# Kernel tuning notes

Hardware: AMD Instinct MI355X
Metric: run time of the kernel (lower is better)

The kernel has to match this reference:

```python
import jax, jax.numpy as jnp
import numpy as np

EMBED_DIM = 64
NUM_HEADS = 8
D_K = EMBED_DIM // NUM_HEADS  # 8
B, S = 8, 1024


def setup_inputs() -> dict:
    key = jax.random.key(0)
    ks = jax.random.split(key, 10)
    f32 = jnp.float32
    lim = 1.0 / np.sqrt(EMBED_DIM)
    def lin(k):
        kw, kb = jax.random.split(k)
        w = jax.random.uniform(kw, (EMBED_DIM, EMBED_DIM), f32, -lim, lim)
        b = jax.random.uniform(kb, (EMBED_DIM,), f32, -lim, lim)
        return w, b
    wq, bq = lin(ks[0])
    wk, bk = lin(ks[1])
    wv, bv = lin(ks[2])
    wo, bo = lin(ks[3])
    theta = jax.random.normal(ks[4], (EMBED_DIM,), f32)  # trainable RY angles, one per wire
    x = jax.random.normal(ks[5], (B, S, EMBED_DIM), f32)
    return {"x": x, "wq": wq, "bq": bq, "wk": wk, "bk": bk,
            "wv": wv, "bv": bv, "theta": theta, "wo": wo, "bo": bo}


def _quantum_map(t, theta):
    # Per-qubit circuit on |0>: RX(t_i) encode, RY(theta_i), <PauliZ_i>.
    # Product state => <Z_i> = cos(theta_i) * cos(t_i) exactly.
    return jnp.cos(theta) * jnp.cos(t.reshape(-1, EMBED_DIM))  # [N, E]


def reference(x, wq, bq, wk, bk, wv, bv, theta, wo, bo):
    # Linear QKV (torch nn.Linear: x @ W^T + b)
    q = x @ wq.T + bq
    k = x @ wk.T + bk
    v = x @ wv.T + bv
    # Quantum measurement map, flattened over batch*seq (as in the original)
    q_q = _quantum_map(q, theta)  # [N, E], N = B*S
    k_q = _quantum_map(k, theta)
    v_q = _quantum_map(v, theta)
    # Full flattened attention: [N, N] scores (original never reshapes back)
    scores = (q_q @ k_q.T) / jnp.sqrt(jnp.asarray(D_K, x.dtype))
    attn = jax.nn.softmax(scores, axis=-1)  # dropout is identity in eval
    out = attn @ v_q  # [N, E]
    return out @ wo.T + bo
```

## Files before the change

kernel.cpp:

```cpp
#include <hip/hip_runtime.h>
#include <hip/hip_bf16.h>

#define NQ 8192
#define DIM 64
#define SPLITS 8
#define QBLK 128
#define BN 64
#define KEYS_PER_SPLIT (NQ / SPLITS)
#define NTILES (KEYS_PER_SPLIT / BN)
#define SCALE 0.35355339059327373f
#define SC2   0.51012301920911057f

#define KSTR 72
#define VSTR 68

typedef short s8v __attribute__((ext_vector_type(8)));
typedef short s4v __attribute__((ext_vector_type(4)));
typedef float f4v __attribute__((ext_vector_type(4)));

__device__ __forceinline__ float b2f(short s) {
  unsigned int u = ((unsigned int)(unsigned short)s) << 16;
  return __uint_as_float(u);
}
__device__ __forceinline__ short f2b(float f) {
  __hip_bfloat16 h = __float2bfloat16(f);
  return *reinterpret_cast<short*>(&h);
}

__device__ __forceinline__ f4v mfma16(s4v a, s4v b, f4v c) {
#if __has_builtin(__builtin_amdgcn_mfma_f32_16x16x16bf16_1k)
  return __builtin_amdgcn_mfma_f32_16x16x16bf16_1k(a, b, c, 0, 0, 0);
#else
  f4v d;
  asm volatile("v_mfma_f32_16x16x16_bf16 %0, %1, %2, %3"
               : "=v"(d) : "v"(a), "v"(b), "v"(c));
  return d;
#endif
}

#define QROWS 16
__global__ __launch_bounds__(256) void qkv_kernel(
    const float* __restrict__ x,
    const float* __restrict__ wq, const float* __restrict__ bq,
    const float* __restrict__ wk, const float* __restrict__ bk,
    const float* __restrict__ wv, const float* __restrict__ bv,
    const float* __restrict__ theta,
    short* __restrict__ qq, short* __restrict__ kq, short* __restrict__ vq) {
  __shared__ __align__(16) short wsh[3][DIM][KSTR];
  __shared__ __align__(16) short xsb[QROWS][DIM];
  int tid = threadIdx.x;
  for (int i = tid; i < 3 * DIM * 16; i += 256) {
    int m = i >> 10;
    int rem = i & 1023;
    int r = rem >> 4, c4 = (rem & 15) << 2;
    const float* src = (m == 0) ? wq : (m == 1) ? wk : wv;
    float4 w = *(const float4*)&src[r * DIM + c4];
    s4v p = {f2b(w.x), f2b(w.y), f2b(w.z), f2b(w.w)};
    *(s4v*)&wsh[m][r][c4] = p;
  }
  int rowbase = blockIdx.x * QROWS;
  for (int i = tid; i < QROWS * 16; i += 256) {
    int r = i >> 4, c4 = (i & 15) << 2;
    float4 v = *(const float4*)&x[(rowbase + r) * DIM + c4];
    s4v p = {f2b(v.x), f2b(v.y), f2b(v.z), f2b(v.w)};
    *(s4v*)&xsb[r][c4] = p;
  }
  __syncthreads();
  int e = tid & 63, rg = tid >> 6;
  float ct = __cosf(theta[e]);
  float bqv = bq[e], bkv = bk[e], bvv = bv[e];
  for (int r = rg; r < QROWS; r += 4) {
    float aq = bqv, ak = bkv, av = bvv;
#pragma unroll
    for (int c8 = 0; c8 < 8; ++c8) {
      s8v xv = *(const s8v*)&xsb[r][c8 * 8];
      s8v w0 = *(const s8v*)&wsh[0][e][c8 * 8];
      s8v w1 = *(const s8v*)&wsh[1][e][c8 * 8];
      s8v w2 = *(const s8v*)&wsh[2][e][c8 * 8];
#pragma unroll
      for (int j = 0; j < 8; ++j) {
        float xf = b2f(xv[j]);
        aq += xf * b2f(w0[j]);
        ak += xf * b2f(w1[j]);
        av += xf * b2f(w2[j]);
      }
    }
    int n = rowbase + r;
    qq[n * DIM + e] = f2b(ct * __cosf(aq));
    kq[n * DIM + e] = f2b(ct * __cosf(ak));
    vq[n * DIM + e] = f2b(ct * __cosf(av));
  }
}

__global__ __launch_bounds__(256) void flash_kernel(
    const short* __restrict__ qq, const short* __restrict__ kq,
    const short* __restrict__ vq,
    float* __restrict__ pO, float* __restrict__ pL) {
  __shared__ __align__(16) short ksh[BN * KSTR];
  __shared__ __align__(16) short vsh[DIM * VSTR];

  int tid = threadIdx.x;
  int wave = tid >> 6, lane = tid & 63;
  int l15 = lane & 15, quad = lane >> 4;
  int qblock = blockIdx.x >> 3, split = blockIdx.x & 7;
  int qbase = qblock * QBLK + wave * 32;

  s8v qf[2][2];
#pragma unroll
  for (int qt = 0; qt < 2; ++qt) {
    const short* qr = qq + (qbase + qt * 16 + l15) * DIM + quad * 8;
    qf[qt][0] = *(const s8v*)qr;
    qf[qt][1] = *(const s8v*)(qr + 32);
  }

  f4v o[2][4];
  float ls[2] = {0.f, 0.f};
#pragma unroll
  for (int qt = 0; qt < 2; ++qt)
#pragma unroll
    for (int c = 0; c < 4; ++c) o[qt][c] = (f4v){0.f, 0.f, 0.f, 0.f};

  int kp = tid & 31, dch = tid >> 5;

  int kstart = split * KEYS_PER_SPLIT;
  for (int t = 0; t < NTILES; ++t) {
    int kbase = kstart + t * BN;
    __syncthreads();
    for (int i = tid; i < 512; i += 256) {
      int key = i >> 3, c8 = (i & 7) << 3;
      *(s8v*)&ksh[key * KSTR + c8] = *(const s8v*)&kq[(kbase + key) * DIM + c8];
    }
    {
      s8v r0 = *(const s8v*)&vq[(kbase + 2 * kp) * DIM + (dch << 3)];
      s8v r1 = *(const s8v*)&vq[(kbase + 2 * kp + 1) * DIM + (dch << 3)];
#pragma unroll
      for (int j = 0; j < 8; ++j) {
        int d = (dch << 3) + j;
        int pk = (int)(unsigned short)r0[j] | ((int)(unsigned short)r1[j] << 16);
        *(int*)&vsh[d * VSTR + 2 * kp] = pk;
      }
    }
    __syncthreads();

#pragma unroll
    for (int kt = 0; kt < 4; ++kt) {
      const short* kr = &ksh[(kt * 16 + l15) * KSTR + quad * 8];
      s8v kf0 = *(const s8v*)kr;
      s8v kf1 = *(const s8v*)(kr + 32);
      s4v pa[2];
#pragma unroll
      for (int qt = 0; qt < 2; ++qt) {
        f4v acc = (f4v){0.f, 0.f, 0.f, 0.f};
        acc = __builtin_amdgcn_mfma_f32_16x16x32_bf16(kf0, qf[qt][0], acc, 0, 0, 0);
        acc = __builtin_amdgcn_mfma_f32_16x16x32_bf16(kf1, qf[qt][1], acc, 0, 0, 0);
        s4v a;
        float sum = 0.f;
#pragma unroll
        for (int r = 0; r < 4; ++r) {
          float p = exp2f(acc[r] * SC2);
          short pb = f2b(p);
          a[r] = pb;
          sum += b2f(pb);
        }
        pa[qt] = a;
        ls[qt] += sum;
      }
#pragma unroll
      for (int c = 0; c < 4; ++c) {
        s4v vf = *(const s4v*)&vsh[(c * 16 + l15) * VSTR + kt * 16 + quad * 4];
#pragma unroll
        for (int qt = 0; qt < 2; ++qt)
          o[qt][c] = mfma16(pa[qt], vf, o[qt][c]);
      }
    }
  }

#pragma unroll
  for (int qt = 0; qt < 2; ++qt) {
    float v = ls[qt];
    v += __shfl_xor(v, 16);
    v += __shfl_xor(v, 32);
    ls[qt] = v;
  }

#pragma unroll
  for (int qt = 0; qt < 2; ++qt) {
#pragma unroll
    for (int r = 0; r < 4; ++r) {
      int q = qbase + qt * 16 + quad * 4 + r;
#pragma unroll
      for (int c = 0; c < 4; ++c)
        pO[((size_t)split * NQ + q) * DIM + c * 16 + l15] = o[qt][c][r];
    }
    if (quad == 0) pL[split * NQ + qbase + qt * 16 + l15] = ls[qt];
  }
}

#define MROWS 8
__global__ __launch_bounds__(256) void merge_kernel(
    const float* __restrict__ pO, const float* __restrict__ pL,
    const float* __restrict__ wo, const float* __restrict__ bo,
    float* __restrict__ out) {
  __shared__ __align__(16) short wsh[DIM][KSTR];
  __shared__ __align__(16) float att[MROWS][DIM];
  int tid = threadIdx.x;
  for (int i = tid; i < DIM * 16; i += 256) {
    int r = i >> 4, c4 = (i & 15) << 2;
    float4 w = *(const float4*)&wo[r * DIM + c4];
    s4v p = {f2b(w.x), f2b(w.y), f2b(w.z), f2b(w.w)};
    *(s4v*)&wsh[r][c4] = p;
  }
  int e = tid & 63, rg = tid >> 6;
  int q0 = blockIdx.x * MROWS;
  for (int rr = rg; rr < MROWS; rr += 4) {
    int q = q0 + rr;
    float s = 0.f, l = 0.f;
#pragma unroll
    for (int sp = 0; sp < SPLITS; ++sp) {
      s += pO[((size_t)sp * NQ + q) * DIM + e];
      l += pL[sp * NQ + q];
    }
    att[rr][e] = s / l;
  }
  __syncthreads();
  for (int rr = rg; rr < MROWS; rr += 4) {
    float acc = bo[e];
#pragma unroll
    for (int c8 = 0; c8 < 8; ++c8) {
      s8v w = *(const s8v*)&wsh[e][c8 * 8];
      float4 a0 = *(const float4*)&att[rr][c8 * 8];
      float4 a1 = *(const float4*)&att[rr][c8 * 8 + 4];
      acc += a0.x * b2f(w[0]) + a0.y * b2f(w[1]) + a0.z * b2f(w[2]) + a0.w * b2f(w[3])
           + a1.x * b2f(w[4]) + a1.y * b2f(w[5]) + a1.z * b2f(w[6]) + a1.w * b2f(w[7]);
    }
    out[(q0 + rr) * DIM + e] = acc;
  }
}

extern "C" void kernel_launch(void* const* d_in, const int* in_sizes, int n_in,
                              void* d_out, int out_size, void* d_ws, size_t ws_size,
                              hipStream_t stream) {
  const float* x  = (const float*)d_in[0];
  const float* wq = (const float*)d_in[1];
  const float* bq = (const float*)d_in[2];
  const float* wk = (const float*)d_in[3];
  const float* bk = (const float*)d_in[4];
  const float* wv = (const float*)d_in[5];
  const float* bv = (const float*)d_in[6];
  const float* th = (const float*)d_in[7];
  const float* wo = (const float*)d_in[8];
  const float* bo = (const float*)d_in[9];

  char* ws = (char*)d_ws;
  short* qq = (short*)(ws);
  short* kq = (short*)(ws + (1u << 20));
  short* vq = (short*)(ws + (2u << 20));
  float* pO = (float*)(ws + (3u << 20));
  float* pL = (float*)(ws + (3u << 20) + (size_t)SPLITS * NQ * DIM * 4);

  hipLaunchKernelGGL(qkv_kernel, dim3(NQ / QROWS), dim3(256), 0, stream,
                     x, wq, bq, wk, bk, wv, bv, th, qq, kq, vq);
  hipLaunchKernelGGL(flash_kernel, dim3((NQ / QBLK) * SPLITS), dim3(256), 0, stream,
                     qq, kq, vq, pO, pL);
  hipLaunchKernelGGL(merge_kernel, dim3(NQ / MROWS), dim3(256), 0, stream,
                     pO, pL, wo, bo, (float*)d_out);
}
```

Before: 134.2 us.

## Fuse merge into flash tail blocks, use bf16 partials, 16 splits, 32-wide PV MFMA

The merge step is folded into the flash kernel: the last TAILB blocks to finish take a ticket from an atomic counter, spin until every block is done, then run the split merge and output projection in place of a separate launch. Partial outputs and row sums are now stored as bf16 instead of fp32, which halves partial traffic at some cost in precision. The key split count doubles to 16 for more parallelism, and the PV product uses the 16x16x32 MFMA with bf16x2 packing instead of 16x16x16. The fused path depends on workspace size and on the spinning tail blocks not starving blocks that have not yet been scheduled.

```diff
diff --git a/kernel.cpp b/kernel.cpp
--- a/kernel.cpp
+++ b/kernel.cpp
@@ -3,13 +3,15 @@
 
 #define NQ 8192
 #define DIM 64
-#define SPLITS 8
+#define SPLITS 16
 #define QBLK 128
 #define BN 64
 #define KEYS_PER_SPLIT (NQ / SPLITS)
 #define NTILES (KEYS_PER_SPLIT / BN)
-#define SCALE 0.35355339059327373f
-#define SC2   0.51012301920911057f
+#define GRID_FLASH ((NQ / QBLK) * SPLITS)
+#define TAILB 256
+#define MROWS 32
+#define SC2 0.51012301920911057f
 
 #define KSTR 72
 #define VSTR 68
@@ -17,6 +19,7 @@
 typedef short s8v __attribute__((ext_vector_type(8)));
 typedef short s4v __attribute__((ext_vector_type(4)));
 typedef float f4v __attribute__((ext_vector_type(4)));
+typedef int   i4v __attribute__((ext_vector_type(4)));
 
 __device__ __forceinline__ float b2f(short s) {
   unsigned int u = ((unsigned int)(unsigned short)s) << 16;
@@ -26,16 +29,10 @@
   __hip_bfloat16 h = __float2bfloat16(f);
   return *reinterpret_cast<short*>(&h);
 }
-
-__device__ __forceinline__ f4v mfma16(s4v a, s4v b, f4v c) {
-#if __has_builtin(__builtin_amdgcn_mfma_f32_16x16x16bf16_1k)
-  return __builtin_amdgcn_mfma_f32_16x16x16bf16_1k(a, b, c, 0, 0, 0);
-#else
-  f4v d;
-  asm volatile("v_mfma_f32_16x16x16_bf16 %0, %1, %2, %3"
-               : "=v"(d) : "v"(a), "v"(b), "v"(c));
-  return d;
-#endif
+__device__ __forceinline__ int pack_bf16x2(float a, float b) {
+  union { __hip_bfloat162 h; int i; } u;
+  u.h = __float22bfloat162_rn(make_float2(a, b));
+  return u.i;
 }
 
 #define QROWS 16
@@ -45,7 +42,10 @@
     const float* __restrict__ wk, const float* __restrict__ bk,
     const float* __restrict__ wv, const float* __restrict__ bv,
     const float* __restrict__ theta,
-    short* __restrict__ qq, short* __restrict__ kq, short* __restrict__ vq) {
+    short* __restrict__ qq, short* __restrict__ kq, short* __restrict__ vq,
+    unsigned int* cnt, int fused) {
+  if (fused && blockIdx.x == 0 && threadIdx.x == 0)
+    __hip_atomic_store(cnt, 0u, __ATOMIC_RELAXED, __HIP_MEMORY_SCOPE_AGENT);
   __shared__ __align__(16) short wsh[3][DIM][KSTR];
   __shared__ __align__(16) short xsb[QROWS][DIM];
   int tid = threadIdx.x;
@@ -92,17 +92,57 @@
   }
 }
 
-__global__ __launch_bounds__(256) void flash_kernel(
+__device__ __forceinline__ void merge_rows(
+    int q0, const short* __restrict__ pO, const short* __restrict__ pL,
+    const float* __restrict__ wo, const float* __restrict__ bo,
+    float* __restrict__ out, short* wsh, float* att) {
+  int tid = threadIdx.x;
+  for (int i = tid; i < DIM * 16; i += 256) {
+    int r = i >> 4, c4 = (i & 15) << 2;
+    float4 w = *(const float4*)&wo[r * DIM + c4];
+    s4v p = {f2b(w.x), f2b(w.y), f2b(w.z), f2b(w.w)};
+    *(s4v*)&wsh[r * KSTR + c4] = p;
+  }
+  int e = tid & 63, rg = tid >> 6;
+  for (int rr = rg; rr < MROWS; rr += 4) {
+    int q = q0 + rr;
+    float s = 0.f, l = 0.f;
+#pragma unroll
+    for (int sp = 0; sp < SPLITS; ++sp) {
+      s += b2f(pO[((size_t)sp * NQ + q) * DIM + e]);
+      l += b2f(pL[sp * NQ + q]);
+    }
+    att[rr * DIM + e] = s / l;
+  }
+  __syncthreads();
+  for (int rr = rg; rr < MROWS; rr += 4) {
+    float acc = bo[e];
+#pragma unroll
+    for (int c8 = 0; c8 < 8; ++c8) {
+      s8v w = *(const s8v*)&wsh[e * KSTR + c8 * 8];
+      const float* ar = &att[rr * DIM + c8 * 8];
+      acc += ar[0] * b2f(w[0]) + ar[1] * b2f(w[1]) + ar[2] * b2f(w[2]) + ar[3] * b2f(w[3])
+           + ar[4] * b2f(w[4]) + ar[5] * b2f(w[5]) + ar[6] * b2f(w[6]) + ar[7] * b2f(w[7]);
+    }
+    out[(size_t)(q0 + rr) * DIM + e] = acc;
+  }
+}
+
+__global__ __launch_bounds__(256, 4) void flash_kernel(
     const short* __restrict__ qq, const short* __restrict__ kq,
     const short* __restrict__ vq,
-    float* __restrict__ pO, float* __restrict__ pL) {
+    short* __restrict__ pO, short* __restrict__ pL,
+    unsigned int* cnt,
+    const float* __restrict__ wo, const float* __restrict__ bo,
+    float* __restrict__ out, int fused) {
   __shared__ __align__(16) short ksh[BN * KSTR];
   __shared__ __align__(16) short vsh[DIM * VSTR];
+  __shared__ unsigned int tkt_s;
 
   int tid = threadIdx.x;
   int wave = tid >> 6, lane = tid & 63;
   int l15 = lane & 15, quad = lane >> 4;
-  int qblock = blockIdx.x >> 3, split = blockIdx.x & 7;
+  int qblock = blockIdx.x >> 4, split = blockIdx.x & 15;
   int qbase = qblock * QBLK + wave * 32;
 
   s8v qf[2][2];
@@ -120,7 +160,7 @@
 #pragma unroll
     for (int c = 0; c < 4; ++c) o[qt][c] = (f4v){0.f, 0.f, 0.f, 0.f};
 
-  int kp = tid & 31, dch = tid >> 5;
+  int vkp = tid & 31, vdc = tid >> 5;
 
   int kstart = split * KEYS_PER_SPLIT;
   for (int t = 0; t < NTILES; ++t) {
@@ -131,46 +171,48 @@
       *(s8v*)&ksh[key * KSTR + c8] = *(const s8v*)&kq[(kbase + key) * DIM + c8];
     }
     {
-      s8v r0 = *(const s8v*)&vq[(kbase + 2 * kp) * DIM + (dch << 3)];
-      s8v r1 = *(const s8v*)&vq[(kbase + 2 * kp + 1) * DIM + (dch << 3)];
+      s8v r0 = *(const s8v*)&vq[(kbase + 2 * vkp) * DIM + (vdc << 3)];
+      s8v r1 = *(const s8v*)&vq[(kbase + 2 * vkp + 1) * DIM + (vdc << 3)];
 #pragma unroll
       for (int j = 0; j < 8; ++j) {
-        int d = (dch << 3) + j;
+        int d = (vdc << 3) + j;
         int pk = (int)(unsigned short)r0[j] | ((int)(unsigned short)r1[j] << 16);
-        *(int*)&vsh[d * VSTR + 2 * kp] = pk;
+        *(int*)&vsh[d * VSTR + 2 * vkp] = pk;
       }
     }
     __syncthreads();
 
 #pragma unroll
-    for (int kt = 0; kt < 4; ++kt) {
-      const short* kr = &ksh[(kt * 16 + l15) * KSTR + quad * 8];
-      s8v kf0 = *(const s8v*)kr;
-      s8v kf1 = *(const s8v*)(kr + 32);
-      s4v pa[2];
-#pragma unroll
-      for (int qt = 0; qt < 2; ++qt) {
-        f4v acc = (f4v){0.f, 0.f, 0.f, 0.f};
-        acc = __builtin_amdgcn_mfma_f32_16x16x32_bf16(kf0, qf[qt][0], acc, 0, 0, 0);
-        acc = __builtin_amdgcn_mfma_f32_16x16x32_bf16(kf1, qf[qt][1], acc, 0, 0, 0);
-        s4v a;
-        float sum = 0.f;
-#pragma unroll
-        for (int r = 0; r < 4; ++r) {
-          float p = exp2f(acc[r] * SC2);
-          short pb = f2b(p);
-          a[r] = pb;
-          sum += b2f(pb);
+    for (int kp = 0; kp < 2; ++kp) {
+      i4v pai[2];
+#pragma unroll
+      for (int h = 0; h < 2; ++h) {
+        int kt = kp * 2 + h;
+        const short* kr = &ksh[(kt * 16 + l15) * KSTR + quad * 8];
+        s8v kf0 = *(const s8v*)kr;
+        s8v kf1 = *(const s8v*)(kr + 32);
+#pragma unroll
+        for (int qt = 0; qt < 2; ++qt) {
+          f4v acc = (f4v){0.f, 0.f, 0.f, 0.f};
+          acc = __builtin_amdgcn_mfma_f32_16x16x32_bf16(kf0, qf[qt][0], acc, 0, 0, 0);
+          acc = __builtin_amdgcn_mfma_f32_16x16x32_bf16(kf1, qf[qt][1], acc, 0, 0, 0);
+          float p0 = exp2f(acc[0] * SC2), p1 = exp2f(acc[1] * SC2);
+          float p2 = exp2f(acc[2] * SC2), p3 = exp2f(acc[3] * SC2);
+          ls[qt] += (p0 + p1) + (p2 + p3);
+          pai[qt][h * 2]     = pack_bf16x2(p0, p1);
+          pai[qt][h * 2 + 1] = pack_bf16x2(p2, p3);
         }
-        pa[qt] = a;
-        ls[qt] += sum;
       }
 #pragma unroll
       for (int c = 0; c < 4; ++c) {
-        s4v vf = *(const s4v*)&vsh[(c * 16 + l15) * VSTR + kt * 16 + quad * 4];
+        const short* vr = &vsh[(c * 16 + l15) * VSTR + kp * 32 + quad * 4];
+        s4v v0 = *(const s4v*)vr;
+        s4v v1 = *(const s4v*)(vr + 16);
+        s8v vf = __builtin_shufflevector(v0, v1, 0, 1, 2, 3, 4, 5, 6, 7);
 #pragma unroll
         for (int qt = 0; qt < 2; ++qt)
-          o[qt][c] = mfma16(pa[qt], vf, o[qt][c]);
+          o[qt][c] = __builtin_amdgcn_mfma_f32_16x16x32_bf16(
+              __builtin_bit_cast(s8v, pai[qt]), vf, o[qt][c], 0, 0, 0);
       }
     }
   }
@@ -188,53 +230,42 @@
 #pragma unroll
     for (int r = 0; r < 4; ++r) {
       int q = qbase + qt * 16 + quad * 4 + r;
+      size_t ob = ((size_t)split * NQ + q) * DIM;
 #pragma unroll
       for (int c = 0; c < 4; ++c)
-        pO[((size_t)split * NQ + q) * DIM + c * 16 + l15] = o[qt][c][r];
-    }
-    if (quad == 0) pL[split * NQ + qbase + qt * 16 + l15] = ls[qt];
-  }
-}
-
-#define MROWS 8
+        pO[ob + c * 16 + l15] = f2b(o[qt][c][r]);
+    }
+    if (quad == 0) pL[split * NQ + qbase + qt * 16 + l15] = f2b(ls[qt]);
+  }
+
+  if (!fused) return;
+
+  __threadfence();
+  __syncthreads();
+  if (tid == 0)
+    tkt_s = __hip_atomic_fetch_add(cnt, 1u, __ATOMIC_ACQ_REL,
+                                   __HIP_MEMORY_SCOPE_AGENT);
+  __syncthreads();
+  unsigned tkt = tkt_s;
+  if (tkt < GRID_FLASH - TAILB) return;
+  if (tid == 0) {
+    while (__hip_atomic_load(cnt, __ATOMIC_ACQUIRE, __HIP_MEMORY_SCOPE_AGENT)
+           < GRID_FLASH)
+      __builtin_amdgcn_s_sleep(2);
+  }
+  __syncthreads();
+  __threadfence();
+  merge_rows((int)(tkt - (GRID_FLASH - TAILB)) * MROWS, pO, pL, wo, bo, out,
+             ksh, (float*)vsh);
+}
+
 __global__ __launch_bounds__(256) void merge_kernel(
-    const float* __restrict__ pO, const float* __restrict__ pL,
+    const short* __restrict__ pO, const short* __restrict__ pL,
     const float* __restrict__ wo, const float* __restrict__ bo,
     float* __restrict__ out) {
-  __shared__ __align__(16) short wsh[DIM][KSTR];
-  __shared__ __align__(16) float att[MROWS][DIM];
-  int tid = threadIdx.x;
-  for (int i = tid; i < DIM * 16; i += 256) {
-    int r = i >> 4, c4 = (i & 15) << 2;
-    float4 w = *(const float4*)&wo[r * DIM + c4];
-    s4v p = {f2b(w.x), f2b(w.y), f2b(w.z), f2b(w.w)};
-    *(s4v*)&wsh[r][c4] = p;
-  }
-  int e = tid & 63, rg = tid >> 6;
-  int q0 = blockIdx.x * MROWS;
-  for (int rr = rg; rr < MROWS; rr += 4) {
-    int q = q0 + rr;
-    float s = 0.f, l = 0.f;
-#pragma unroll
-    for (int sp = 0; sp < SPLITS; ++sp) {
-      s += pO[((size_t)sp * NQ + q) * DIM + e];
-      l += pL[sp * NQ + q];
-    }
-    att[rr][e] = s / l;
-  }
-  __syncthreads();
-  for (int rr = rg; rr < MROWS; rr += 4) {
-    float acc = bo[e];
-#pragma unroll
-    for (int c8 = 0; c8 < 8; ++c8) {
-      s8v w = *(const s8v*)&wsh[e][c8 * 8];
-      float4 a0 = *(const float4*)&att[rr][c8 * 8];
-      float4 a1 = *(const float4*)&att[rr][c8 * 8 + 4];
-      acc += a0.x * b2f(w[0]) + a0.y * b2f(w[1]) + a0.z * b2f(w[2]) + a0.w * b2f(w[3])
-           + a1.x * b2f(w[4]) + a1.y * b2f(w[5]) + a1.z * b2f(w[6]) + a1.w * b2f(w[7]);
-    }
-    out[(q0 + rr) * DIM + e] = acc;
-  }
+  __shared__ __align__(16) short wsh[DIM * KSTR];
+  __shared__ __align__(16) float att[MROWS * DIM];
+  merge_rows(blockIdx.x * MROWS, pO, pL, wo, bo, out, wsh, att);
 }
 
 extern "C" void kernel_launch(void* const* d_in, const int* in_sizes, int n_in,
@@ -255,13 +286,16 @@
   short* qq = (short*)(ws);
   short* kq = (short*)(ws + (1u << 20));
   short* vq = (short*)(ws + (2u << 20));
-  float* pO = (float*)(ws + (3u << 20));
-  float* pL = (float*)(ws + (3u << 20) + (size_t)SPLITS * NQ * DIM * 4);
+  short* pO = (short*)(ws + (3u << 20));
+  short* pL = (short*)(ws + (19u << 20));
+  unsigned int* cnt = (unsigned int*)(ws + (19u << 20) + (256u << 10));
+  int fused = ws_size >= ((19u << 20) + (256u << 10) + 4u);
 
   hipLaunchKernelGGL(qkv_kernel, dim3(NQ / QROWS), dim3(256), 0, stream,
-                     x, wq, bq, wk, bk, wv, bv, th, qq, kq, vq);
-  hipLaunchKernelGGL(flash_kernel, dim3((NQ / QBLK) * SPLITS), dim3(256), 0, stream,
-                     qq, kq, vq, pO, pL);
-  hipLaunchKernelGGL(merge_kernel, dim3(NQ / MROWS), dim3(256), 0, stream,
-                     pO, pL, wo, bo, (float*)d_out);
-}
+                     x, wq, bq, wk, bk, wv, bv, th, qq, kq, vq, cnt, fused);
+  hipLaunchKernelGGL(flash_kernel, dim3(GRID_FLASH), dim3(256), 0, stream,
+                     qq, kq, vq, pO, pL, cnt, wo, bo, (float*)d_out, fused);
+  if (!fused)
+    hipLaunchKernelGGL(merge_kernel, dim3(NQ / MROWS), dim3(256), 0, stream,
+                       pO, pL, wo, bo, (float*)d_out);
+}
```

New measurement: 338.7 us. 2.52x slower.
